# Performance work log

Hardware: AMD Instinct MI355X
Metric: run time of the kernel (lower is better)

The kernel has to match this reference:

```python
import jax, jax.numpy as jnp
import numpy as np

T, B, I, H, O = 2048, 16, 256, 256, 8


def setup_inputs() -> dict:
    key = jax.random.key(0)
    ks = jax.random.split(key, 7)
    return {
        "x": jax.random.normal(ks[0], (T, B, I), dtype=jnp.float32),
        "noise": jax.random.normal(ks[1], (T, B, H, O), dtype=jnp.float32),
        "sigma_rec": jax.random.uniform(ks[2], (H, O), dtype=jnp.float32),
        "B_w": jax.random.normal(ks[3], (O, H, I), dtype=jnp.float32) / np.float32(np.sqrt(I)),
        "B_b": jax.random.normal(ks[4], (O, H), dtype=jnp.float32) * 0.01,
        "W_w": jax.random.normal(ks[5], (O, H), dtype=jnp.float32) / np.float32(np.sqrt(H)),
        "W_b": jax.random.normal(ks[6], (O,), dtype=jnp.float32) * 0.01,
        "alpha": jnp.float32(1.0),  # RNN.__init__ hard-codes alpha = 1
    }


def reference(x, noise, sigma_rec, B_w, B_b, W_w, W_b, alpha):
    # Precompute all per-channel input projections as one batched GEMM:
    # total_input[t,b,h,o] = input2hs[o](x[t,b])  -> (T, B, H, O)
    tot = jnp.einsum('tbi,ohi->tbho', x, B_w) + B_b.T  # B_b.T: (H, O)

    def step(state, inp):
        ti, nz = inp  # (B,H,O) each
        new_state = alpha * (ti - state) + state + sigma_rec * nz
        return new_state, jnp.tanh(new_state)

    state0 = jnp.zeros((x.shape[1], H, O), dtype=x.dtype)
    _, rnn_activity = jax.lax.scan(step, state0, (tot, noise))  # (T,B,H,O)

    # Per-channel readout: fcs[o] applied to rnn_activity[..., o]
    out = jnp.einsum('tbho,oh->tbo', rnn_activity, W_w) + W_b  # (T,B,O)
    return out, rnn_activity
```

## Files before the change

### kernel.cpp

```cpp
#include <hip/hip_runtime.h>
#include <hip/hip_bf16.h>

#define TT     2048
#define BBATCH 16
#define IDIM   256
#define HDIM   256
#define ODIM   8
#define MM (TT * BBATCH)
#define NN (HDIM * ODIM)
#define KK IDIM
#define NBLK (NN / 128)

typedef __attribute__((ext_vector_type(8))) short bf16x8;
typedef __attribute__((ext_vector_type(4))) float f32x4;
typedef unsigned int u32;

__device__ __forceinline__ unsigned short f2bfu(float f) {
  __hip_bfloat16 h = __float2bfloat16(f);
  return *reinterpret_cast<unsigned short*>(&h);
}

__device__ __forceinline__ float fast_tanh(float x) {
  float a = __builtin_fabsf(x);
  float t = __expf(-2.0f * a);
  float r = __fdividef(1.0f - t, 1.0f + t);
  return __builtin_copysignf(r, x);
}

__device__ __forceinline__ void gload16(const void* g, void* l) {
  __builtin_amdgcn_global_load_lds((const __attribute__((address_space(1))) u32*)g,
                                   (__attribute__((address_space(3))) u32*)l, 16, 0, 0);
}

__global__ __launch_bounds__(256) void conv_x_kernel(const float* __restrict__ x,
                                                     unsigned short* __restrict__ xb) {
  size_t id = (size_t)blockIdx.x * 256 + threadIdx.x;
  int m = (int)(id >> 6);
  int g = (int)(id & 63);
  float4 v = reinterpret_cast<const float4*>(x)[id];
  ushort4 o;
  o.x = f2bfu(v.x); o.y = f2bfu(v.y); o.z = f2bfu(v.z); o.w = f2bfu(v.w);
  int dstbyte = (g * 8) ^ ((m & 7) << 4);
  *reinterpret_cast<ushort4*>(xb + (size_t)m * KK + dstbyte / 2) = o;
}

__global__ __launch_bounds__(64) void conv_w_kernel(const float* __restrict__ Bw,
                                                    const float* __restrict__ Bb,
                                                    const float* __restrict__ Ww,
                                                    unsigned short* __restrict__ wb,
                                                    float* __restrict__ biasn,
                                                    float* __restrict__ wwn) {
  int n = blockIdx.x;
  int j = threadIdx.x;
  int o = n & 7, h = n >> 3;
  const float* src = Bw + ((size_t)o * HDIM + h) * IDIM;
  float4 v = reinterpret_cast<const float4*>(src)[j];
  ushort4 p;
  p.x = f2bfu(v.x); p.y = f2bfu(v.y); p.z = f2bfu(v.z); p.w = f2bfu(v.w);
  int dstbyte = (j * 8) ^ ((n & 7) << 4);
  *reinterpret_cast<ushort4*>(wb + (size_t)n * KK + dstbyte / 2) = p;
  if (j == 0) biasn[n] = Bb[o * HDIM + h];
  if (j == 32) wwn[n] = Ww[o * HDIM + h];
}

template <bool FUSE>
__global__ __launch_bounds__(256, 2) void gemm_lds_kernel(
    const unsigned short* __restrict__ xb, const unsigned short* __restrict__ wb,
    const float* __restrict__ biasn, const float* __restrict__ wwn,
    const float* __restrict__ noise, const float* __restrict__ sigma,
    const float* __restrict__ alphap,
    float* __restrict__ act, float* __restrict__ partial) {
  __shared__ __align__(16) char lds[65536];

  const int tid = threadIdx.x;
  const int l = tid & 63;
  const int w = tid >> 6;
  const int wr = w >> 1, wc = w & 1;
  const int mbase = blockIdx.y * 128, nbase = blockIdx.x * 128;
  const int m0 = mbase + wr * 64, n0 = nbase + wc * 64;
  const int lr = l & 15, lg = l >> 4;
  const float alpha = alphap[0];

  float4 nz[4][4], sg4[4], bs4[4];
#pragma unroll
  for (int ni = 0; ni < 4; ++ni) {
    sg4[ni] = *reinterpret_cast<const float4*>(sigma + n0 + ni * 16 + lg * 4);
    bs4[ni] = *reinterpret_cast<const float4*>(biasn + n0 + ni * 16 + lg * 4);
  }
#pragma unroll
  for (int mi = 0; mi < 4; ++mi) {
    const float* nrow = noise + (size_t)(m0 + mi * 16 + lr) * NN + n0 + lg * 4;
#pragma unroll
    for (int ni = 0; ni < 4; ++ni)
      nz[mi][ni] = *reinterpret_cast<const float4*>(nrow + ni * 16);
  }
  asm volatile("" ::: "memory");

  const int srow = w * 32 + (l >> 3);
  const int spb = (l & 7) * 16;

  f32x4 acc[4][4];
#pragma unroll
  for (int ni = 0; ni < 4; ++ni)
#pragma unroll
    for (int mi = 0; mi < 4; ++mi) acc[ni][mi] = (f32x4){0.f, 0.f, 0.f, 0.f};

  auto STAGE = [&](int buf, int s) {
    const char* gA = (const char*)xb + (size_t)(mbase + srow) * 512 + s * 128 + spb;
    const char* gB = (const char*)wb + (size_t)(nbase + srow) * 512 + s * 128 + spb;
    char* lA = lds + buf * 16384 + w * 4096;
    char* lB = lds + 32768 + buf * 16384 + w * 4096;
#pragma unroll
    for (int r = 0; r < 4; ++r) gload16(gA + (size_t)r * 8 * 512, lA + r * 1024);
#pragma unroll
    for (int r = 0; r < 4; ++r) gload16(gB + (size_t)r * 8 * 512, lB + r * 1024);
  };

  const int swz = (lr & 7) << 4;
  auto COMPUTE = [&](int buf) {
    const char* lA = lds + buf * 16384;
    const char* lB = lds + 32768 + buf * 16384;
#pragma unroll
    for (int kc = 0; kc < 2; ++kc) {
      const int cbs = (kc * 64 + lg * 16) ^ swz;
      bf16x8 a[4], b[4];
#pragma unroll
      for (int mi = 0; mi < 4; ++mi)
        a[mi] = *reinterpret_cast<const bf16x8*>(lA + (wr * 64 + mi * 16 + lr) * 128 + cbs);
#pragma unroll
      for (int ni = 0; ni < 4; ++ni)
        b[ni] = *reinterpret_cast<const bf16x8*>(lB + (wc * 64 + ni * 16 + lr) * 128 + cbs);
#pragma unroll
      for (int ni = 0; ni < 4; ++ni)
#pragma unroll
        for (int mi = 0; mi < 4; ++mi)
          acc[ni][mi] = __builtin_amdgcn_mfma_f32_16x16x32_bf16(b[ni], a[mi], acc[ni][mi], 0, 0, 0);
    }
  };

  STAGE(0, 0);
#pragma unroll
  for (int s = 0; s < 4; ++s) {
    if (s < 3) {
      STAGE((s + 1) & 1, s + 1);
      asm volatile("s_waitcnt vmcnt(8)" ::: "memory");
    } else {
      asm volatile("s_waitcnt vmcnt(0)" ::: "memory");
    }
    __builtin_amdgcn_s_barrier();
    COMPUTE(s & 1);
    __builtin_amdgcn_s_barrier();
  }

  if (alpha == 1.0f) {
    float4 ww4[4];
    f32x4 pp[4];
#pragma unroll
    for (int ni = 0; ni < 4; ++ni)
      ww4[ni] = *reinterpret_cast<const float4*>(wwn + n0 + ni * 16 + lg * 4);
#pragma unroll
    for (int mi = 0; mi < 4; ++mi) pp[mi] = (f32x4){0.f, 0.f, 0.f, 0.f};

#pragma unroll
    for (int mi = 0; mi < 4; ++mi) {
      float* arow = act + (size_t)(m0 + mi * 16 + lr) * NN + n0 + lg * 4;
#pragma unroll
      for (int ni = 0; ni < 4; ++ni) {
        float4 v;
        v.x = fast_tanh(acc[ni][mi][0] + bs4[ni].x + sg4[ni].x * nz[mi][ni].x);
        v.y = fast_tanh(acc[ni][mi][1] + bs4[ni].y + sg4[ni].y * nz[mi][ni].y);
        v.z = fast_tanh(acc[ni][mi][2] + bs4[ni].z + sg4[ni].z * nz[mi][ni].z);
        v.w = fast_tanh(acc[ni][mi][3] + bs4[ni].w + sg4[ni].w * nz[mi][ni].w);
        *reinterpret_cast<float4*>(arow + ni * 16) = v;
        if constexpr (FUSE) {
          pp[mi][0] += v.x * ww4[ni].x;
          pp[mi][1] += v.y * ww4[ni].y;
          pp[mi][2] += v.z * ww4[ni].z;
          pp[mi][3] += v.w * ww4[ni].w;
        }
      }
    }

    if constexpr (FUSE) {
      f32x4* red = reinterpret_cast<f32x4*>(lds);
      __syncthreads();
#pragma unroll
      for (int mi = 0; mi < 4; ++mi)
        red[((w * 4 + mi) * 16 + lr) * 4 + lg] = pp[mi];
      __syncthreads();
      const int t = tid;
      const int wr2 = t >> 7, mi2 = (t >> 5) & 3, lr2 = (t >> 1) & 15, oh = t & 1;
      f32x4 s0 = red[(((wr2 * 2 + 0) * 4 + mi2) * 16 + lr2) * 4 + oh];
      f32x4 s1 = red[(((wr2 * 2 + 0) * 4 + mi2) * 16 + lr2) * 4 + oh + 2];
      f32x4 s2 = red[(((wr2 * 2 + 1) * 4 + mi2) * 16 + lr2) * 4 + oh];
      f32x4 s3 = red[(((wr2 * 2 + 1) * 4 + mi2) * 16 + lr2) * 4 + oh + 2];
      f32x4 sm = s0 + s1 + s2 + s3;
      const int m = mbase + wr2 * 64 + mi2 * 16 + lr2;
      float4 outv = {sm[0], sm[1], sm[2], sm[3]};
      *reinterpret_cast<float4*>(partial + ((size_t)m * NBLK + blockIdx.x) * 8 + oh * 4) = outv;
    }
  } else {
#pragma unroll
    for (int mi = 0; mi < 4; ++mi) {
      float* arow = act + (size_t)(m0 + mi * 16 + lr) * NN + n0 + lg * 4;
#pragma unroll
      for (int ni = 0; ni < 4; ++ni) {
        float4 v;
        v.x = acc[ni][mi][0] + bs4[ni].x;
        v.y = acc[ni][mi][1] + bs4[ni].y;
        v.z = acc[ni][mi][2] + bs4[ni].z;
        v.w = acc[ni][mi][3] + bs4[ni].w;
        *reinterpret_cast<float4*>(arow + ni * 16) = v;
      }
    }
  }
}

__global__ __launch_bounds__(256) void reduce_kernel(const float* __restrict__ partial,
                                                     const float* __restrict__ Wb,
                                                     const float* __restrict__ alphap,
                                                     float* __restrict__ out) {
  if (alphap[0] != 1.0f) return;
  const int gid = blockIdx.x * 256 + threadIdx.x;
  const int m = gid >> 1, oh = gid & 1;
  const float4 wb4 = *reinterpret_cast<const float4*>(Wb + oh * 4);
  float4 s = {wb4.x, wb4.y, wb4.z, wb4.w};
  const float* p = partial + (size_t)m * NBLK * 8 + oh * 4;
#pragma unroll
  for (int nb = 0; nb < NBLK; ++nb) {
    const float4 v = *reinterpret_cast<const float4*>(p + nb * 8);
    s.x += v.x; s.y += v.y; s.z += v.z; s.w += v.w;
  }
  *reinterpret_cast<float4*>(out + (size_t)m * ODIM + oh * 4) = s;
}

__global__ __launch_bounds__(256) void gemm_direct_kernel(
    const float* __restrict__ xf, const float* __restrict__ Bw, const float* __restrict__ Bb,
    const float* __restrict__ noise, const float* __restrict__ sigma,
    const float* __restrict__ alphap,
    float* __restrict__ act) {
  const int tid = threadIdx.x;
  const int l = tid & 63;
  const int w = tid >> 6;
  const int wr = w >> 1, wc = w & 1;
  const int m0 = blockIdx.y * 128 + wr * 64;
  const int n0 = blockIdx.x * 128 + wc * 64;
  const int lr = l & 15, lg = l >> 4;

  f32x4 acc[4][4];
#pragma unroll
  for (int ni = 0; ni < 4; ++ni)
#pragma unroll
    for (int mi = 0; mi < 4; ++mi) acc[ni][mi] = (f32x4){0.f, 0.f, 0.f, 0.f};

#pragma unroll
  for (int kt = 0; kt < KK / 32; ++kt) {
    const int kk = kt * 32 + lg * 8;
    bf16x8 a[4], b[4];
#pragma unroll
    for (int mi = 0; mi < 4; ++mi) {
      const float* ap = xf + (size_t)(m0 + mi * 16 + lr) * KK + kk;
      float4 u0 = *reinterpret_cast<const float4*>(ap);
      float4 u1 = *reinterpret_cast<const float4*>(ap + 4);
      bf16x8 t;
      t[0] = (short)f2bfu(u0.x); t[1] = (short)f2bfu(u0.y);
      t[2] = (short)f2bfu(u0.z); t[3] = (short)f2bfu(u0.w);
      t[4] = (short)f2bfu(u1.x); t[5] = (short)f2bfu(u1.y);
      t[6] = (short)f2bfu(u1.z); t[7] = (short)f2bfu(u1.w);
      a[mi] = t;
    }
#pragma unroll
    for (int ni = 0; ni < 4; ++ni) {
      int n = n0 + ni * 16 + lr;
      const float* wp = Bw + ((size_t)(n & 7) * HDIM + (n >> 3)) * IDIM + kk;
      float4 u0 = *reinterpret_cast<const float4*>(wp);
      float4 u1 = *reinterpret_cast<const float4*>(wp + 4);
      bf16x8 t;
      t[0] = (short)f2bfu(u0.x); t[1] = (short)f2bfu(u0.y);
      t[2] = (short)f2bfu(u0.z); t[3] = (short)f2bfu(u0.w);
      t[4] = (short)f2bfu(u1.x); t[5] = (short)f2bfu(u1.y);
      t[6] = (short)f2bfu(u1.z); t[7] = (short)f2bfu(u1.w);
      b[ni] = t;
    }
#pragma unroll
    for (int ni = 0; ni < 4; ++ni)
#pragma unroll
      for (int mi = 0; mi < 4; ++mi)
        acc[ni][mi] = __builtin_amdgcn_mfma_f32_16x16x32_bf16(b[ni], a[mi], acc[ni][mi], 0, 0, 0);
  }

  const float alpha = alphap[0];
#pragma unroll
  for (int mi = 0; mi < 4; ++mi) {
    const int m = m0 + mi * 16 + lr;
    const float* nrow = noise + (size_t)m * NN;
    float* arow = act + (size_t)m * NN;
#pragma unroll
    for (int ni = 0; ni < 4; ++ni) {
      const int n = n0 + ni * 16 + lg * 4;
      const float4 sg = *reinterpret_cast<const float4*>(sigma + n);
      float4 bs;
      bs.x = Bb[((n + 0) & 7) * HDIM + ((n + 0) >> 3)];
      bs.y = Bb[((n + 1) & 7) * HDIM + ((n + 1) >> 3)];
      bs.z = Bb[((n + 2) & 7) * HDIM + ((n + 2) >> 3)];
      bs.w = Bb[((n + 3) & 7) * HDIM + ((n + 3) >> 3)];
      const float4 nzv = *reinterpret_cast<const float4*>(nrow + n);
      float4 v;
      v.x = acc[ni][mi][0] + bs.x;
      v.y = acc[ni][mi][1] + bs.y;
      v.z = acc[ni][mi][2] + bs.z;
      v.w = acc[ni][mi][3] + bs.w;
      if (alpha == 1.0f) {
        v.x = fast_tanh(v.x + sg.x * nzv.x);
        v.y = fast_tanh(v.y + sg.y * nzv.y);
        v.z = fast_tanh(v.z + sg.z * nzv.z);
        v.w = fast_tanh(v.w + sg.w * nzv.w);
      }
      *reinterpret_cast<float4*>(arow + n) = v;
    }
  }
}

__global__ __launch_bounds__(256) void scan_kernel(const float* __restrict__ noise,
                                                   const float* __restrict__ sigma,
                                                   const float* __restrict__ alphap,
                                                   float* __restrict__ act) {
  const float alpha = alphap[0];
  if (alpha == 1.0f) return;
  const int id = blockIdx.x * 256 + threadIdx.x;
  const int b = id >> 11;
  const int n = id & (NN - 1);
  const float sg = sigma[n];
  float s = 0.f;
  for (int t = 0; t < TT; ++t) {
    const size_t idx = ((size_t)(t * BBATCH + b)) * NN + n;
    const float tot = act[idx];
    const float ns = alpha * (tot - s) + s + sg * noise[idx];
    act[idx] = tanhf(ns);
    s = ns;
  }
}

__global__ __launch_bounds__(256) void readout_kernel(const float* __restrict__ act,
                                                      const float* __restrict__ Ww,
                                                      const float* __restrict__ Wb,
                                                      const float* __restrict__ alphap,
                                                      int fused,
                                                      float* __restrict__ out) {
  if (fused && alphap[0] == 1.0f) return;
  __shared__ float red[256][9];
  const int m = blockIdx.x;
  const int j = threadIdx.x;
  const float4 v0 = *reinterpret_cast<const float4*>(act + (size_t)m * NN + j * 8);
  const float4 v1 = *reinterpret_cast<const float4*>(act + (size_t)m * NN + j * 8 + 4);
  float av[8] = {v0.x, v0.y, v0.z, v0.w, v1.x, v1.y, v1.z, v1.w};
#pragma unroll
  for (int o = 0; o < 8; ++o) red[j][o] = av[o] * Ww[o * HDIM + j];
  __syncthreads();
  for (int s = 128; s >= 1; s >>= 1) {
    if (j < s) {
#pragma unroll
      for (int o = 0; o < 8; ++o) red[j][o] += red[j + s][o];
    }
    __syncthreads();
  }
  if (j < 8) out[(size_t)m * ODIM + j] = red[0][j] + Wb[j];
}

extern "C" void kernel_launch(void* const* d_in, const int* in_sizes, int n_in,
                              void* d_out, int out_size, void* d_ws, size_t ws_size,
                              hipStream_t stream) {
  const float* x     = (const float*)d_in[0];
  const float* noise = (const float*)d_in[1];
  const float* sigma = (const float*)d_in[2];
  const float* Bw    = (const float*)d_in[3];
  const float* Bb    = (const float*)d_in[4];
  const float* Ww    = (const float*)d_in[5];
  const float* Wb    = (const float*)d_in[6];
  const float* alpha = (const float*)d_in[7];

  float* out = (float*)d_out;
  float* act = out + (size_t)TT * BBATCH * ODIM;

  const size_t xb_bytes = (size_t)MM * KK * 2;
  const size_t wb_bytes = (size_t)NN * KK * 2;
  const size_t bias_bytes = (size_t)NN * 4;
  const size_t wwn_bytes = (size_t)NN * 4;
  const size_t part_bytes = (size_t)MM * NBLK * 8 * 4;
  const size_t need_prep = xb_bytes + wb_bytes + bias_bytes + wwn_bytes;
  const size_t need_fuse = need_prep + part_bytes;
  const bool prep = ws_size >= need_prep;
  const bool fuse = ws_size >= need_fuse;

  unsigned short* xb = (unsigned short*)d_ws;
  unsigned short* wb = (unsigned short*)((char*)d_ws + xb_bytes);
  float* biasn = (float*)((char*)d_ws + xb_bytes + wb_bytes);
  float* wwn   = (float*)((char*)d_ws + xb_bytes + wb_bytes + bias_bytes);
  float* part  = (float*)((char*)d_ws + need_prep);

  dim3 grid(NN / 128, MM / 128);
  if (prep) {
    conv_x_kernel<<<(MM * KK / 4) / 256, 256, 0, stream>>>(x, xb);
    conv_w_kernel<<<NN, 64, 0, stream>>>(Bw, Bb, Ww, wb, biasn, wwn);
    if (fuse) {
      gemm_lds_kernel<true><<<grid, 256, 0, stream>>>(xb, wb, biasn, wwn, noise, sigma,
                                                      alpha, act, part);
    } else {
      gemm_lds_kernel<false><<<grid, 256, 0, stream>>>(xb, wb, biasn, wwn, noise, sigma,
                                                       alpha, act, nullptr);
    }
  } else {
    gemm_direct_kernel<<<grid, 256, 0, stream>>>(x, Bw, Bb, noise, sigma, alpha, act);
  }

  scan_kernel<<<(BBATCH * NN) / 256, 256, 0, stream>>>(noise, sigma, alpha, act);
  if (fuse) {
    reduce_kernel<<<MM * 2 / 256, 256, 0, stream>>>(part, Wb, alpha, out);
  }
  readout_kernel<<<MM, 256, 0, stream>>>(act, Ww, Wb, alpha, fuse ? 1 : 0, out);
}
```

Before: 166.8 us.

## Halve GEMM LDS footprint and defer noise loads to raise occupancy

The GEMM now stages K in eight 32-element slices instead of four 64-element slices. This halves the shared-memory buffer to 32KB, and the x and weight swizzles are narrowed to match the 64-byte row pitch. The noise, sigma and bias register prefetch moves from before the main loop into the epilogue, and launch bounds rise to 3 blocks per CU. The aim is more resident waves to hide memory latency in this bandwidth-bound tanh/readout kernel, at the cost of exposing the noise load latency at the end and running more, shorter pipeline stages with more barriers.

```diff
diff --git a/kernel.cpp b/kernel.cpp
--- a/kernel.cpp
+++ b/kernel.cpp
@@ -40,7 +40,7 @@
   float4 v = reinterpret_cast<const float4*>(x)[id];
   ushort4 o;
   o.x = f2bfu(v.x); o.y = f2bfu(v.y); o.z = f2bfu(v.z); o.w = f2bfu(v.w);
-  int dstbyte = (g * 8) ^ ((m & 7) << 4);
+  int dstbyte = (g * 8) ^ ((m & 3) << 4);
   *reinterpret_cast<ushort4*>(xb + (size_t)m * KK + dstbyte / 2) = o;
 }
 
@@ -57,20 +57,20 @@
   float4 v = reinterpret_cast<const float4*>(src)[j];
   ushort4 p;
   p.x = f2bfu(v.x); p.y = f2bfu(v.y); p.z = f2bfu(v.z); p.w = f2bfu(v.w);
-  int dstbyte = (j * 8) ^ ((n & 7) << 4);
+  int dstbyte = (j * 8) ^ ((n & 3) << 4);
   *reinterpret_cast<ushort4*>(wb + (size_t)n * KK + dstbyte / 2) = p;
   if (j == 0) biasn[n] = Bb[o * HDIM + h];
   if (j == 32) wwn[n] = Ww[o * HDIM + h];
 }
 
 template <bool FUSE>
-__global__ __launch_bounds__(256, 2) void gemm_lds_kernel(
+__global__ __launch_bounds__(256, 3) void gemm_lds_kernel(
     const unsigned short* __restrict__ xb, const unsigned short* __restrict__ wb,
     const float* __restrict__ biasn, const float* __restrict__ wwn,
     const float* __restrict__ noise, const float* __restrict__ sigma,
     const float* __restrict__ alphap,
     float* __restrict__ act, float* __restrict__ partial) {
-  __shared__ __align__(16) char lds[65536];
+  __shared__ __align__(16) char lds[32768];
 
   const int tid = threadIdx.x;
   const int l = tid & 63;
@@ -81,96 +81,90 @@
   const int lr = l & 15, lg = l >> 4;
   const float alpha = alphap[0];
 
-  float4 nz[4][4], sg4[4], bs4[4];
-#pragma unroll
-  for (int ni = 0; ni < 4; ++ni) {
-    sg4[ni] = *reinterpret_cast<const float4*>(sigma + n0 + ni * 16 + lg * 4);
-    bs4[ni] = *reinterpret_cast<const float4*>(biasn + n0 + ni * 16 + lg * 4);
-  }
-#pragma unroll
-  for (int mi = 0; mi < 4; ++mi) {
-    const float* nrow = noise + (size_t)(m0 + mi * 16 + lr) * NN + n0 + lg * 4;
+  f32x4 acc[4][4];
+#pragma unroll
+  for (int ni = 0; ni < 4; ++ni)
+#pragma unroll
+    for (int mi = 0; mi < 4; ++mi) acc[ni][mi] = (f32x4){0.f, 0.f, 0.f, 0.f};
+
+  const int srow = (l >> 2);
+  const int schk = (l & 3) * 16;
+
+  auto STAGE = [&](int buf, int s) {
+    const int kb = s * 64;
+#pragma unroll
+    for (int r = 0; r < 2; ++r) {
+      const int row = w * 32 + r * 16 + srow;
+      const char* gA = (const char*)xb + (size_t)(mbase + row) * 512 + kb + schk;
+      gload16(gA, lds + buf * 8192 + (w * 32 + r * 16) * 64);
+    }
+#pragma unroll
+    for (int r = 0; r < 2; ++r) {
+      const int row = w * 32 + r * 16 + srow;
+      const char* gB = (const char*)wb + (size_t)(nbase + row) * 512 + kb + schk;
+      gload16(gB, lds + 16384 + buf * 8192 + (w * 32 + r * 16) * 64);
+    }
+  };
+
+  const int cswz = (lr & 3) << 4;
+  auto COMPUTE = [&](int buf) {
+    const char* lA = lds + buf * 8192;
+    const char* lB = lds + 16384 + buf * 8192;
+    const int cbs = (lg * 16) ^ cswz;
+    bf16x8 a[4], b[4];
+#pragma unroll
+    for (int mi = 0; mi < 4; ++mi)
+      a[mi] = *reinterpret_cast<const bf16x8*>(lA + (wr * 64 + mi * 16 + lr) * 64 + cbs);
 #pragma unroll
     for (int ni = 0; ni < 4; ++ni)
-      nz[mi][ni] = *reinterpret_cast<const float4*>(nrow + ni * 16);
-  }
-  asm volatile("" ::: "memory");
-
-  const int srow = w * 32 + (l >> 3);
-  const int spb = (l & 7) * 16;
-
-  f32x4 acc[4][4];
-#pragma unroll
-  for (int ni = 0; ni < 4; ++ni)
-#pragma unroll
-    for (int mi = 0; mi < 4; ++mi) acc[ni][mi] = (f32x4){0.f, 0.f, 0.f, 0.f};
-
-  auto STAGE = [&](int buf, int s) {
-    const char* gA = (const char*)xb + (size_t)(mbase + srow) * 512 + s * 128 + spb;
-    const char* gB = (const char*)wb + (size_t)(nbase + srow) * 512 + s * 128 + spb;
-    char* lA = lds + buf * 16384 + w * 4096;
-    char* lB = lds + 32768 + buf * 16384 + w * 4096;
-#pragma unroll
-    for (int r = 0; r < 4; ++r) gload16(gA + (size_t)r * 8 * 512, lA + r * 1024);
-#pragma unroll
-    for (int r = 0; r < 4; ++r) gload16(gB + (size_t)r * 8 * 512, lB + r * 1024);
+      b[ni] = *reinterpret_cast<const bf16x8*>(lB + (wc * 64 + ni * 16 + lr) * 64 + cbs);
+#pragma unroll
+    for (int ni = 0; ni < 4; ++ni)
+#pragma unroll
+      for (int mi = 0; mi < 4; ++mi)
+        acc[ni][mi] = __builtin_amdgcn_mfma_f32_16x16x32_bf16(b[ni], a[mi], acc[ni][mi], 0, 0, 0);
   };
 
-  const int swz = (lr & 7) << 4;
-  auto COMPUTE = [&](int buf) {
-    const char* lA = lds + buf * 16384;
-    const char* lB = lds + 32768 + buf * 16384;
-#pragma unroll
-    for (int kc = 0; kc < 2; ++kc) {
-      const int cbs = (kc * 64 + lg * 16) ^ swz;
-      bf16x8 a[4], b[4];
-#pragma unroll
-      for (int mi = 0; mi < 4; ++mi)
-        a[mi] = *reinterpret_cast<const bf16x8*>(lA + (wr * 64 + mi * 16 + lr) * 128 + cbs);
-#pragma unroll
-      for (int ni = 0; ni < 4; ++ni)
-        b[ni] = *reinterpret_cast<const bf16x8*>(lB + (wc * 64 + ni * 16 + lr) * 128 + cbs);
-#pragma unroll
-      for (int ni = 0; ni < 4; ++ni)
-#pragma unroll
-        for (int mi = 0; mi < 4; ++mi)
-          acc[ni][mi] = __builtin_amdgcn_mfma_f32_16x16x32_bf16(b[ni], a[mi], acc[ni][mi], 0, 0, 0);
-    }
-  };
-
   STAGE(0, 0);
-#pragma unroll
-  for (int s = 0; s < 4; ++s) {
-    if (s < 3) {
-      STAGE((s + 1) & 1, s + 1);
-      asm volatile("s_waitcnt vmcnt(8)" ::: "memory");
-    } else {
-      asm volatile("s_waitcnt vmcnt(0)" ::: "memory");
-    }
+  STAGE(1, 1);
+#pragma unroll
+  for (int s = 0; s < 8; ++s) {
+    if (s < 7) asm volatile("s_waitcnt vmcnt(4)" ::: "memory");
+    else       asm volatile("s_waitcnt vmcnt(0)" ::: "memory");
     __builtin_amdgcn_s_barrier();
     COMPUTE(s & 1);
     __builtin_amdgcn_s_barrier();
+    if (s + 2 < 8) STAGE(s & 1, s + 2);
   }
 
   if (alpha == 1.0f) {
-    float4 ww4[4];
+    float4 sg4[4], bs4[4], ww4[4];
+#pragma unroll
+    for (int ni = 0; ni < 4; ++ni) {
+      sg4[ni] = *reinterpret_cast<const float4*>(sigma + n0 + ni * 16 + lg * 4);
+      bs4[ni] = *reinterpret_cast<const float4*>(biasn + n0 + ni * 16 + lg * 4);
+      if constexpr (FUSE)
+        ww4[ni] = *reinterpret_cast<const float4*>(wwn + n0 + ni * 16 + lg * 4);
+    }
     f32x4 pp[4];
 #pragma unroll
-    for (int ni = 0; ni < 4; ++ni)
-      ww4[ni] = *reinterpret_cast<const float4*>(wwn + n0 + ni * 16 + lg * 4);
-#pragma unroll
     for (int mi = 0; mi < 4; ++mi) pp[mi] = (f32x4){0.f, 0.f, 0.f, 0.f};
 
 #pragma unroll
     for (int mi = 0; mi < 4; ++mi) {
+      const float* nrow = noise + (size_t)(m0 + mi * 16 + lr) * NN + n0 + lg * 4;
       float* arow = act + (size_t)(m0 + mi * 16 + lr) * NN + n0 + lg * 4;
+      float4 nzv[4];
+#pragma unroll
+      for (int ni = 0; ni < 4; ++ni)
+        nzv[ni] = *reinterpret_cast<const float4*>(nrow + ni * 16);
 #pragma unroll
       for (int ni = 0; ni < 4; ++ni) {
         float4 v;
-        v.x = fast_tanh(acc[ni][mi][0] + bs4[ni].x + sg4[ni].x * nz[mi][ni].x);
-        v.y = fast_tanh(acc[ni][mi][1] + bs4[ni].y + sg4[ni].y * nz[mi][ni].y);
-        v.z = fast_tanh(acc[ni][mi][2] + bs4[ni].z + sg4[ni].z * nz[mi][ni].z);
-        v.w = fast_tanh(acc[ni][mi][3] + bs4[ni].w + sg4[ni].w * nz[mi][ni].w);
+        v.x = fast_tanh(acc[ni][mi][0] + bs4[ni].x + sg4[ni].x * nzv[ni].x);
+        v.y = fast_tanh(acc[ni][mi][1] + bs4[ni].y + sg4[ni].y * nzv[ni].y);
+        v.z = fast_tanh(acc[ni][mi][2] + bs4[ni].z + sg4[ni].z * nzv[ni].z);
+        v.w = fast_tanh(acc[ni][mi][3] + bs4[ni].w + sg4[ni].w * nzv[ni].w);
         *reinterpret_cast<float4*>(arow + ni * 16) = v;
         if constexpr (FUSE) {
           pp[mi][0] += v.x * ww4[ni].x;
@@ -200,6 +194,10 @@
       *reinterpret_cast<float4*>(partial + ((size_t)m * NBLK + blockIdx.x) * 8 + oh * 4) = outv;
     }
   } else {
+    float4 bs4[4];
+#pragma unroll
+    for (int ni = 0; ni < 4; ++ni)
+      bs4[ni] = *reinterpret_cast<const float4*>(biasn + n0 + ni * 16 + lg * 4);
 #pragma unroll
     for (int mi = 0; mi < 4; ++mi) {
       float* arow = act + (size_t)(m0 + mi * 16 + lr) * NN + n0 + lg * 4;
```

Measured after the change: 235.4 us. +41.1%, slower.

## Single-buffer LDS, defer noise loads to epilogue, raise occupancy to four blocks

Applied to the files above, without the earlier changes.

The GEMM kernel drops LDS double buffering (64KB to 32KB) and loads noise, sigma and bias in the epilogue instead of holding 64 noise floats in registers through the main loop. The launch bound is raised to four blocks per CU. A touch-prefetch of noise at kernel start is meant to warm the cache. This gives up overlap of global loads with MFMA inside each block in exchange for more resident blocks hiding latency, with register pressure as the main risk.

```diff
diff --git a/kernel.cpp b/kernel.cpp
--- a/kernel.cpp
+++ b/kernel.cpp
@@ -64,13 +64,13 @@
 }
 
 template <bool FUSE>
-__global__ __launch_bounds__(256, 2) void gemm_lds_kernel(
+__global__ __launch_bounds__(256, 4) void gemm_lds_kernel(
     const unsigned short* __restrict__ xb, const unsigned short* __restrict__ wb,
     const float* __restrict__ biasn, const float* __restrict__ wwn,
     const float* __restrict__ noise, const float* __restrict__ sigma,
     const float* __restrict__ alphap,
     float* __restrict__ act, float* __restrict__ partial) {
-  __shared__ __align__(16) char lds[65536];
+  __shared__ __align__(16) char lds[32768];
 
   const int tid = threadIdx.x;
   const int l = tid & 63;
@@ -81,35 +81,29 @@
   const int lr = l & 15, lg = l >> 4;
   const float alpha = alphap[0];
 
-  float4 nz[4][4], sg4[4], bs4[4];
-#pragma unroll
-  for (int ni = 0; ni < 4; ++ni) {
-    sg4[ni] = *reinterpret_cast<const float4*>(sigma + n0 + ni * 16 + lg * 4);
-    bs4[ni] = *reinterpret_cast<const float4*>(biasn + n0 + ni * 16 + lg * 4);
-  }
-#pragma unroll
-  for (int mi = 0; mi < 4; ++mi) {
-    const float* nrow = noise + (size_t)(m0 + mi * 16 + lr) * NN + n0 + lg * 4;
-#pragma unroll
-    for (int ni = 0; ni < 4; ++ni)
-      nz[mi][ni] = *reinterpret_cast<const float4*>(nrow + ni * 16);
-  }
-  asm volatile("" ::: "memory");
+  {
+    const int i0 = tid, i1 = tid + 256;
+    const float* t0 = noise + (size_t)(mbase + (i0 >> 2)) * NN + nbase + (i0 & 3) * 32;
+    const float* t1 = noise + (size_t)(mbase + (i1 >> 2)) * NN + nbase + (i1 & 3) * 32;
+    f32x4 a = *reinterpret_cast<const f32x4*>(t0);
+    f32x4 b = *reinterpret_cast<const f32x4*>(t1);
+    asm volatile("" :: "v"(a), "v"(b));
+  }
+
+  f32x4 acc[4][4];
+#pragma unroll
+  for (int ni = 0; ni < 4; ++ni)
+#pragma unroll
+    for (int mi = 0; mi < 4; ++mi) acc[ni][mi] = (f32x4){0.f, 0.f, 0.f, 0.f};
 
   const int srow = w * 32 + (l >> 3);
   const int spb = (l & 7) * 16;
 
-  f32x4 acc[4][4];
-#pragma unroll
-  for (int ni = 0; ni < 4; ++ni)
-#pragma unroll
-    for (int mi = 0; mi < 4; ++mi) acc[ni][mi] = (f32x4){0.f, 0.f, 0.f, 0.f};
-
-  auto STAGE = [&](int buf, int s) {
+  auto STAGE = [&](int s) {
     const char* gA = (const char*)xb + (size_t)(mbase + srow) * 512 + s * 128 + spb;
     const char* gB = (const char*)wb + (size_t)(nbase + srow) * 512 + s * 128 + spb;
-    char* lA = lds + buf * 16384 + w * 4096;
-    char* lB = lds + 32768 + buf * 16384 + w * 4096;
+    char* lA = lds + w * 4096;
+    char* lB = lds + 16384 + w * 4096;
 #pragma unroll
     for (int r = 0; r < 4; ++r) gload16(gA + (size_t)r * 8 * 512, lA + r * 1024);
 #pragma unroll
@@ -117,9 +111,9 @@
   };
 
   const int swz = (lr & 7) << 4;
-  auto COMPUTE = [&](int buf) {
-    const char* lA = lds + buf * 16384;
-    const char* lB = lds + 32768 + buf * 16384;
+  auto COMPUTE = [&]() {
+    const char* lA = lds;
+    const char* lB = lds + 16384;
 #pragma unroll
     for (int kc = 0; kc < 2; ++kc) {
       const int cbs = (kc * 64 + lg * 16) ^ swz;
@@ -138,39 +132,42 @@
     }
   };
 
-  STAGE(0, 0);
 #pragma unroll
   for (int s = 0; s < 4; ++s) {
-    if (s < 3) {
-      STAGE((s + 1) & 1, s + 1);
-      asm volatile("s_waitcnt vmcnt(8)" ::: "memory");
-    } else {
-      asm volatile("s_waitcnt vmcnt(0)" ::: "memory");
-    }
-    __builtin_amdgcn_s_barrier();
-    COMPUTE(s & 1);
-    __builtin_amdgcn_s_barrier();
+    STAGE(s);
+    __syncthreads();
+    COMPUTE();
+    __syncthreads();
   }
 
   if (alpha == 1.0f) {
-    float4 ww4[4];
+    float4 sg4[4], bs4[4], ww4[4];
+#pragma unroll
+    for (int ni = 0; ni < 4; ++ni) {
+      sg4[ni] = *reinterpret_cast<const float4*>(sigma + n0 + ni * 16 + lg * 4);
+      bs4[ni] = *reinterpret_cast<const float4*>(biasn + n0 + ni * 16 + lg * 4);
+      if constexpr (FUSE)
+        ww4[ni] = *reinterpret_cast<const float4*>(wwn + n0 + ni * 16 + lg * 4);
+    }
     f32x4 pp[4];
 #pragma unroll
-    for (int ni = 0; ni < 4; ++ni)
-      ww4[ni] = *reinterpret_cast<const float4*>(wwn + n0 + ni * 16 + lg * 4);
-#pragma unroll
     for (int mi = 0; mi < 4; ++mi) pp[mi] = (f32x4){0.f, 0.f, 0.f, 0.f};
 
 #pragma unroll
     for (int mi = 0; mi < 4; ++mi) {
+      const float* nrow = noise + (size_t)(m0 + mi * 16 + lr) * NN + n0 + lg * 4;
       float* arow = act + (size_t)(m0 + mi * 16 + lr) * NN + n0 + lg * 4;
+      float4 nzv[4];
+#pragma unroll
+      for (int ni = 0; ni < 4; ++ni)
+        nzv[ni] = *reinterpret_cast<const float4*>(nrow + ni * 16);
 #pragma unroll
       for (int ni = 0; ni < 4; ++ni) {
         float4 v;
-        v.x = fast_tanh(acc[ni][mi][0] + bs4[ni].x + sg4[ni].x * nz[mi][ni].x);
-        v.y = fast_tanh(acc[ni][mi][1] + bs4[ni].y + sg4[ni].y * nz[mi][ni].y);
-        v.z = fast_tanh(acc[ni][mi][2] + bs4[ni].z + sg4[ni].z * nz[mi][ni].z);
-        v.w = fast_tanh(acc[ni][mi][3] + bs4[ni].w + sg4[ni].w * nz[mi][ni].w);
+        v.x = fast_tanh(acc[ni][mi][0] + bs4[ni].x + sg4[ni].x * nzv[ni].x);
+        v.y = fast_tanh(acc[ni][mi][1] + bs4[ni].y + sg4[ni].y * nzv[ni].y);
+        v.z = fast_tanh(acc[ni][mi][2] + bs4[ni].z + sg4[ni].z * nzv[ni].z);
+        v.w = fast_tanh(acc[ni][mi][3] + bs4[ni].w + sg4[ni].w * nzv[ni].w);
         *reinterpret_cast<float4*>(arow + ni * 16) = v;
         if constexpr (FUSE) {
           pp[mi][0] += v.x * ww4[ni].x;
@@ -200,6 +197,10 @@
       *reinterpret_cast<float4*>(partial + ((size_t)m * NBLK + blockIdx.x) * 8 + oh * 4) = outv;
     }
   } else {
+    float4 bs4[4];
+#pragma unroll
+    for (int ni = 0; ni < 4; ++ni)
+      bs4[ni] = *reinterpret_cast<const float4*>(biasn + n0 + ni * 16 + lg * 4);
 #pragma unroll
     for (int mi = 0; mi < 4; ++mi) {
       float* arow = act + (size_t)(m0 + mi * 16 + lr) * NN + n0 + lg * 4;
```

After: 224.2 us. 34.4% more time.

## Halve GEMM M-tile to 64 rows and defer noise loads to epilogue

Applied to the files above, without the earlier changes.

Shrinks the fused GEMM block tile from 128x128 to 64x128, cutting LDS to 48KB and per-thread accumulators so three blocks can fit per CU and twice as many blocks are launched. Instead of holding noise in registers through the main loop, it issues a prefetch of noise into cache at the start and reloads it in the epilogue, along with sigma and bias. This is meant to raise occupancy and lower register pressure, at the cost of less B-tile reuse (B is restaged twice as often) and a second read of noise that depends on it still being in cache.

```diff
diff --git a/kernel.cpp b/kernel.cpp
--- a/kernel.cpp
+++ b/kernel.cpp
@@ -64,76 +64,77 @@
 }
 
 template <bool FUSE>
-__global__ __launch_bounds__(256, 2) void gemm_lds_kernel(
+__global__ __launch_bounds__(256, 3) void gemm_lds_kernel(
     const unsigned short* __restrict__ xb, const unsigned short* __restrict__ wb,
     const float* __restrict__ biasn, const float* __restrict__ wwn,
     const float* __restrict__ noise, const float* __restrict__ sigma,
     const float* __restrict__ alphap,
     float* __restrict__ act, float* __restrict__ partial) {
-  __shared__ __align__(16) char lds[65536];
+  __shared__ __align__(16) char lds[49152];
 
   const int tid = threadIdx.x;
   const int l = tid & 63;
   const int w = tid >> 6;
   const int wr = w >> 1, wc = w & 1;
-  const int mbase = blockIdx.y * 128, nbase = blockIdx.x * 128;
-  const int m0 = mbase + wr * 64, n0 = nbase + wc * 64;
+  const int mbase = blockIdx.y * 64, nbase = blockIdx.x * 128;
+  const int m0 = mbase + wr * 32, n0 = nbase + wc * 64;
   const int lr = l & 15, lg = l >> 4;
   const float alpha = alphap[0];
 
-  float4 nz[4][4], sg4[4], bs4[4];
-#pragma unroll
-  for (int ni = 0; ni < 4; ++ni) {
-    sg4[ni] = *reinterpret_cast<const float4*>(sigma + n0 + ni * 16 + lg * 4);
-    bs4[ni] = *reinterpret_cast<const float4*>(biasn + n0 + ni * 16 + lg * 4);
-  }
-#pragma unroll
-  for (int mi = 0; mi < 4; ++mi) {
-    const float* nrow = noise + (size_t)(m0 + mi * 16 + lr) * NN + n0 + lg * 4;
-#pragma unroll
-    for (int ni = 0; ni < 4; ++ni)
-      nz[mi][ni] = *reinterpret_cast<const float4*>(nrow + ni * 16);
-  }
-  asm volatile("" ::: "memory");
-
-  const int srow = w * 32 + (l >> 3);
+  {
+#pragma unroll
+    for (int mi = 0; mi < 2; ++mi) {
+      const float* nrow = noise + (size_t)(m0 + mi * 16 + lr) * NN + n0 + lg * 4;
+#pragma unroll
+      for (int ni = 0; ni < 4; ++ni) {
+        f32x4 t = *reinterpret_cast<const f32x4*>(nrow + ni * 16);
+        asm volatile("" :: "v"(t));
+      }
+    }
+  }
+
+  f32x4 acc[4][2];
+#pragma unroll
+  for (int ni = 0; ni < 4; ++ni)
+#pragma unroll
+    for (int mi = 0; mi < 2; ++mi) acc[ni][mi] = (f32x4){0.f, 0.f, 0.f, 0.f};
+
+  const int srow8 = l >> 3;
   const int spb = (l & 7) * 16;
 
-  f32x4 acc[4][4];
-#pragma unroll
-  for (int ni = 0; ni < 4; ++ni)
-#pragma unroll
-    for (int mi = 0; mi < 4; ++mi) acc[ni][mi] = (f32x4){0.f, 0.f, 0.f, 0.f};
-
   auto STAGE = [&](int buf, int s) {
-    const char* gA = (const char*)xb + (size_t)(mbase + srow) * 512 + s * 128 + spb;
-    const char* gB = (const char*)wb + (size_t)(nbase + srow) * 512 + s * 128 + spb;
-    char* lA = lds + buf * 16384 + w * 4096;
-    char* lB = lds + 32768 + buf * 16384 + w * 4096;
-#pragma unroll
-    for (int r = 0; r < 4; ++r) gload16(gA + (size_t)r * 8 * 512, lA + r * 1024);
-#pragma unroll
-    for (int r = 0; r < 4; ++r) gload16(gB + (size_t)r * 8 * 512, lB + r * 1024);
+#pragma unroll
+    for (int r = 0; r < 2; ++r) {
+      const int row = w * 16 + r * 8 + srow8;
+      gload16((const char*)xb + (size_t)(mbase + row) * 512 + s * 128 + spb,
+              lds + buf * 8192 + (w * 16 + r * 8) * 128);
+    }
+#pragma unroll
+    for (int r = 0; r < 4; ++r) {
+      const int row = w * 32 + r * 8 + srow8;
+      gload16((const char*)wb + (size_t)(nbase + row) * 512 + s * 128 + spb,
+              lds + 16384 + buf * 16384 + (w * 32 + r * 8) * 128);
+    }
   };
 
   const int swz = (lr & 7) << 4;
   auto COMPUTE = [&](int buf) {
-    const char* lA = lds + buf * 16384;
-    const char* lB = lds + 32768 + buf * 16384;
+    const char* lA = lds + buf * 8192;
+    const char* lB = lds + 16384 + buf * 16384;
 #pragma unroll
     for (int kc = 0; kc < 2; ++kc) {
       const int cbs = (kc * 64 + lg * 16) ^ swz;
-      bf16x8 a[4], b[4];
-#pragma unroll
-      for (int mi = 0; mi < 4; ++mi)
-        a[mi] = *reinterpret_cast<const bf16x8*>(lA + (wr * 64 + mi * 16 + lr) * 128 + cbs);
+      bf16x8 a[2], b[4];
+#pragma unroll
+      for (int mi = 0; mi < 2; ++mi)
+        a[mi] = *reinterpret_cast<const bf16x8*>(lA + (wr * 32 + mi * 16 + lr) * 128 + cbs);
 #pragma unroll
       for (int ni = 0; ni < 4; ++ni)
         b[ni] = *reinterpret_cast<const bf16x8*>(lB + (wc * 64 + ni * 16 + lr) * 128 + cbs);
 #pragma unroll
       for (int ni = 0; ni < 4; ++ni)
 #pragma unroll
-        for (int mi = 0; mi < 4; ++mi)
+        for (int mi = 0; mi < 2; ++mi)
           acc[ni][mi] = __builtin_amdgcn_mfma_f32_16x16x32_bf16(b[ni], a[mi], acc[ni][mi], 0, 0, 0);
     }
   };
@@ -143,7 +144,7 @@
   for (int s = 0; s < 4; ++s) {
     if (s < 3) {
       STAGE((s + 1) & 1, s + 1);
-      asm volatile("s_waitcnt vmcnt(8)" ::: "memory");
+      asm volatile("s_waitcnt vmcnt(6)" ::: "memory");
     } else {
       asm volatile("s_waitcnt vmcnt(0)" ::: "memory");
     }
@@ -153,24 +154,33 @@
   }
 
   if (alpha == 1.0f) {
-    float4 ww4[4];
-    f32x4 pp[4];
-#pragma unroll
-    for (int ni = 0; ni < 4; ++ni)
-      ww4[ni] = *reinterpret_cast<const float4*>(wwn + n0 + ni * 16 + lg * 4);
-#pragma unroll
-    for (int mi = 0; mi < 4; ++mi) pp[mi] = (f32x4){0.f, 0.f, 0.f, 0.f};
-
-#pragma unroll
-    for (int mi = 0; mi < 4; ++mi) {
+    float4 sg4[4], bs4[4], ww4[4];
+#pragma unroll
+    for (int ni = 0; ni < 4; ++ni) {
+      sg4[ni] = *reinterpret_cast<const float4*>(sigma + n0 + ni * 16 + lg * 4);
+      bs4[ni] = *reinterpret_cast<const float4*>(biasn + n0 + ni * 16 + lg * 4);
+      if constexpr (FUSE)
+        ww4[ni] = *reinterpret_cast<const float4*>(wwn + n0 + ni * 16 + lg * 4);
+    }
+    f32x4 pp[2];
+#pragma unroll
+    for (int mi = 0; mi < 2; ++mi) pp[mi] = (f32x4){0.f, 0.f, 0.f, 0.f};
+
+#pragma unroll
+    for (int mi = 0; mi < 2; ++mi) {
+      const float* nrow = noise + (size_t)(m0 + mi * 16 + lr) * NN + n0 + lg * 4;
       float* arow = act + (size_t)(m0 + mi * 16 + lr) * NN + n0 + lg * 4;
+      float4 nzv[4];
+#pragma unroll
+      for (int ni = 0; ni < 4; ++ni)
+        nzv[ni] = *reinterpret_cast<const float4*>(nrow + ni * 16);
 #pragma unroll
       for (int ni = 0; ni < 4; ++ni) {
         float4 v;
-        v.x = fast_tanh(acc[ni][mi][0] + bs4[ni].x + sg4[ni].x * nz[mi][ni].x);
-        v.y = fast_tanh(acc[ni][mi][1] + bs4[ni].y + sg4[ni].y * nz[mi][ni].y);
-        v.z = fast_tanh(acc[ni][mi][2] + bs4[ni].z + sg4[ni].z * nz[mi][ni].z);
-        v.w = fast_tanh(acc[ni][mi][3] + bs4[ni].w + sg4[ni].w * nz[mi][ni].w);
+        v.x = fast_tanh(acc[ni][mi][0] + bs4[ni].x + sg4[ni].x * nzv[ni].x);
+        v.y = fast_tanh(acc[ni][mi][1] + bs4[ni].y + sg4[ni].y * nzv[ni].y);
+        v.z = fast_tanh(acc[ni][mi][2] + bs4[ni].z + sg4[ni].z * nzv[ni].z);
+        v.w = fast_tanh(acc[ni][mi][3] + bs4[ni].w + sg4[ni].w * nzv[ni].w);
         *reinterpret_cast<float4*>(arow + ni * 16) = v;
         if constexpr (FUSE) {
           pp[mi][0] += v.x * ww4[ni].x;
@@ -185,23 +195,29 @@
       f32x4* red = reinterpret_cast<f32x4*>(lds);
       __syncthreads();
 #pragma unroll
-      for (int mi = 0; mi < 4; ++mi)
-        red[((w * 4 + mi) * 16 + lr) * 4 + lg] = pp[mi];
+      for (int mi = 0; mi < 2; ++mi)
+        red[((w * 2 + mi) * 16 + lr) * 4 + lg] = pp[mi];
       __syncthreads();
       const int t = tid;
-      const int wr2 = t >> 7, mi2 = (t >> 5) & 3, lr2 = (t >> 1) & 15, oh = t & 1;
-      f32x4 s0 = red[(((wr2 * 2 + 0) * 4 + mi2) * 16 + lr2) * 4 + oh];
-      f32x4 s1 = red[(((wr2 * 2 + 0) * 4 + mi2) * 16 + lr2) * 4 + oh + 2];
-      f32x4 s2 = red[(((wr2 * 2 + 1) * 4 + mi2) * 16 + lr2) * 4 + oh];
-      f32x4 s3 = red[(((wr2 * 2 + 1) * 4 + mi2) * 16 + lr2) * 4 + oh + 2];
-      f32x4 sm = s0 + s1 + s2 + s3;
-      const int m = mbase + wr2 * 64 + mi2 * 16 + lr2;
-      float4 outv = {sm[0], sm[1], sm[2], sm[3]};
-      *reinterpret_cast<float4*>(partial + ((size_t)m * NBLK + blockIdx.x) * 8 + oh * 4) = outv;
+      if (t < 128) {
+        const int wr2 = (t >> 6) & 1, mi2 = (t >> 5) & 1, lr2 = (t >> 1) & 15, oh = t & 1;
+        f32x4 s0 = red[(((wr2 * 2 + 0) * 2 + mi2) * 16 + lr2) * 4 + oh];
+        f32x4 s1 = red[(((wr2 * 2 + 0) * 2 + mi2) * 16 + lr2) * 4 + oh + 2];
+        f32x4 s2 = red[(((wr2 * 2 + 1) * 2 + mi2) * 16 + lr2) * 4 + oh];
+        f32x4 s3 = red[(((wr2 * 2 + 1) * 2 + mi2) * 16 + lr2) * 4 + oh + 2];
+        f32x4 sm = s0 + s1 + s2 + s3;
+        const int m = mbase + wr2 * 32 + mi2 * 16 + lr2;
+        float4 outv = {sm[0], sm[1], sm[2], sm[3]};
+        *reinterpret_cast<float4*>(partial + ((size_t)m * NBLK + blockIdx.x) * 8 + oh * 4) = outv;
+      }
     }
   } else {
-#pragma unroll
-    for (int mi = 0; mi < 4; ++mi) {
+    float4 bs4[4];
+#pragma unroll
+    for (int ni = 0; ni < 4; ++ni)
+      bs4[ni] = *reinterpret_cast<const float4*>(biasn + n0 + ni * 16 + lg * 4);
+#pragma unroll
+    for (int mi = 0; mi < 2; ++mi) {
       float* arow = act + (size_t)(m0 + mi * 16 + lr) * NN + n0 + lg * 4;
 #pragma unroll
       for (int ni = 0; ni < 4; ++ni) {
@@ -398,10 +414,10 @@
   float* wwn   = (float*)((char*)d_ws + xb_bytes + wb_bytes + bias_bytes);
   float* part  = (float*)((char*)d_ws + need_prep);
 
-  dim3 grid(NN / 128, MM / 128);
   if (prep) {
     conv_x_kernel<<<(MM * KK / 4) / 256, 256, 0, stream>>>(x, xb);
     conv_w_kernel<<<NN, 64, 0, stream>>>(Bw, Bb, Ww, wb, biasn, wwn);
+    dim3 grid(NN / 128, MM / 64);
     if (fuse) {
       gemm_lds_kernel<true><<<grid, 256, 0, stream>>>(xb, wb, biasn, wwn, noise, sigma,
                                                       alpha, act, part);
@@ -410,6 +426,7 @@
                                                        alpha, act, nullptr);
     }
   } else {
+    dim3 grid(NN / 128, MM / 128);
     gemm_direct_kernel<<<grid, 256, 0, stream>>>(x, Bw, Bb, noise, sigma, alpha, act);
   }
 
```

After: 228.3 us. 1.37x slower.
